# Performance work log

Hardware: AMD Instinct MI355X
Metric: run time of the kernel (lower is better)

## Reference

```python
import jax, jax.numpy as jnp
import numpy as np

B = 4096          # batch
F = 1024          # feature_count * embedding_dim
E = 16            # embedding_dim (domain embedding)
D = 8             # num_domains
T = F + E         # cross-net total dim
L = 3             # cross layers
EPS = 1e-5


def setup_inputs() -> dict:
    key = jax.random.key(0)
    ks = jax.random.split(key, 32)
    s = 0.02
    inp = {}
    inp["x"] = jax.random.normal(ks[0], (B, F), dtype=jnp.float32)
    inp["domain_ids"] = jax.random.randint(ks[1], (B,), 0, D)
    # partitioned normalization params
    inp["pn_weight"] = jnp.ones((D, F), jnp.float32)
    inp["pn_bias"] = jnp.zeros((D, F), jnp.float32)
    # domain embedding table
    inp["dom_emb"] = jax.random.normal(ks[2], (D, E), jnp.float32) * 0.1
    # cross network: L layers, each Linear(T->1, no bias) + additive bias vector
    inp["cross_w"] = jax.random.normal(ks[3], (L, T), jnp.float32) * s
    inp["cross_b"] = jnp.zeros((L, T), jnp.float32)
    # center MLP: T->512->256->128 (ReLU, ReLU, none)
    inp["cW1"] = jax.random.normal(ks[4], (T, 512), jnp.float32) * s
    inp["cb1"] = jnp.zeros((512,), jnp.float32)
    inp["cW2"] = jax.random.normal(ks[5], (512, 256), jnp.float32) * s
    inp["cb2"] = jnp.zeros((256,), jnp.float32)
    inp["cW3"] = jax.random.normal(ks[6], (256, 128), jnp.float32) * s
    inp["cb3"] = jnp.zeros((128,), jnp.float32)
    # per-domain nets: T->512->256->128; last bias initialized to domain_net_init_bias=1.0
    inp["dW1"] = jax.random.normal(ks[7], (D, T, 512), jnp.float32) * s
    inp["db1"] = jnp.zeros((D, 512), jnp.float32)
    inp["dW2"] = jax.random.normal(ks[8], (D, 512, 256), jnp.float32) * s
    inp["db2"] = jnp.zeros((D, 256), jnp.float32)
    inp["dW3"] = jax.random.normal(ks[9], (D, 256, 128), jnp.float32) * s
    inp["db3"] = jnp.ones((D, 128), jnp.float32)
    # final MLP: 128->64->1
    inp["fW1"] = jax.random.normal(ks[10], (128, 64), jnp.float32) * s
    inp["fb1"] = jnp.zeros((64,), jnp.float32)
    inp["fW2"] = jax.random.normal(ks[11], (64, 1), jnp.float32) * s
    inp["fb2"] = jnp.zeros((1,), jnp.float32)
    # auxiliary net: E->32->1
    inp["aW1"] = jax.random.normal(ks[12], (E, 32), jnp.float32) * s
    inp["ab1"] = jnp.zeros((32,), jnp.float32)
    inp["aW2"] = jax.random.normal(ks[13], (32, 1), jnp.float32) * s
    inp["ab2"] = jnp.zeros((1,), jnp.float32)
    return inp


def _forward(x, domain_ids, pn_weight, pn_bias, dom_emb, cross_w, cross_b,
             cW1, cb1, cW2, cb2, cW3, cb3,
             dW1, db1, dW2, db2, dW3, db3,
             fW1, fb1, fW2, fb2, aW1, ab1, aW2, ab2):
    # --- PartitionedNormalization: per-sample LayerNorm stats + domain-indexed affine ---
    mean = jnp.mean(x, axis=1, keepdims=True)
    var = jnp.mean((x - mean) ** 2, axis=1, keepdims=True)  # unbiased=False
    normed = (x - mean) / jnp.sqrt(var + EPS)
    normed = normed * pn_weight[domain_ids] + pn_bias[domain_ids]

    xd = dom_emb[domain_ids]                    # (B, E)
    x0 = jnp.concatenate([normed, xd], axis=1)  # (B, T)

    # --- CrossNetworkWithDomain ---
    xc = x0
    for i in range(L):
        proj = xc @ cross_w[i]                  # (B,)
        xc = x0 * proj[:, None] + cross_b[i] + xc

    # --- center MLP ---
    h = jax.nn.relu(xc @ cW1 + cb1)
    h = jax.nn.relu(h @ cW2 + cb2)
    h_center = h @ cW3 + cb3                    # (B, 128)

    # --- domain-specific nets: run all D nets, select per-sample ---
    a = jax.nn.relu(jnp.einsum('bi,dio->bdo', xc, dW1) + db1[None])   # (B, D, 512)
    a = jax.nn.relu(jnp.einsum('bdi,dio->bdo', a, dW2) + db2[None])   # (B, D, 256)
    a = jnp.einsum('bdi,dio->bdo', a, dW3) + db3[None]                # (B, D, 128)
    h_domain = a[jnp.arange(a.shape[0]), domain_ids]                  # (B, 128)

    # --- STAR fusion (tanh) ---
    fused = h_center * jnp.tanh(h_domain)

    # --- final MLP + auxiliary net ---
    main_logits = jax.nn.relu(fused @ fW1 + fb1) @ fW2 + fb2          # (B, 1)
    aux_logits = jax.nn.relu(xd @ aW1 + ab1) @ aW2 + ab2              # (B, 1)
    return jax.nn.sigmoid(main_logits + aux_logits)


def reference(x, domain_ids, pn_weight, pn_bias, dom_emb, cross_w, cross_b,
              cW1, cb1, cW2, cb2, cW3, cb3,
              dW1, db1, dW2, db2, dW3, db3,
              fW1, fb1, fW2, fb2, aW1, ab1, aW2, ab2):
    return _forward(x, domain_ids, pn_weight, pn_bias, dom_emb, cross_w, cross_b,
                    cW1, cb1, cW2, cb2, cW3, cb3,
                    dW1, db1, dW2, db2, dW3, db3,
                    fW1, fb1, fW2, fb2, aW1, ab1, aW2, ab2)
```

## Files before the change

kernel.cpp:

```cpp
#include <hip/hip_runtime.h>
#include <math.h>
#include <stdint.h>

#define BATCH 4096
#define FEAT  1024
#define EDIM  16
#define NDOM  8
#define TDIM  1040
#define KP1   1088
#define NLAYER 3
#define EPSV  1e-5f

typedef __attribute__((ext_vector_type(8))) short bf16x8;
typedef __attribute__((ext_vector_type(4))) float f32x4;

__device__ __forceinline__ unsigned short f2bf(float f) {
    union { float f; unsigned int u; } v; v.f = f;
    unsigned int u = v.u;
    return (unsigned short)((u + 0x7fffu + ((u >> 16) & 1u)) >> 16);
}
__device__ __forceinline__ float bf2f(unsigned short u) {
    union { unsigned int u; float f; } v; v.u = ((unsigned int)u) << 16; return v.f;
}
__device__ __forceinline__ void gload_lds16(const void* g, void* l) {
    __builtin_amdgcn_global_load_lds(
        (const __attribute__((address_space(1))) void*)(g),
        (__attribute__((address_space(3))) void*)(l), 16, 0, 0);
}

#define T_W1 136
#define T_W2 32
#define T_W3 8
#define NCONV (T_W1*9 + T_W2*9 + T_W3*9)

__global__ __launch_bounds__(256) void convert_group(
    const int* __restrict__ dom, int* __restrict__ perm, int* __restrict__ starts,
    const float* __restrict__ cW1, const float* __restrict__ dW1,
    const float* __restrict__ cW2, const float* __restrict__ dW2,
    const float* __restrict__ cW3, const float* __restrict__ dW3,
    unsigned short* __restrict__ Wc1b, unsigned short* __restrict__ Wd1b,
    unsigned short* __restrict__ Wc2b, unsigned short* __restrict__ Wd2b,
    unsigned short* __restrict__ Wc3b, unsigned short* __restrict__ Wd3b) {
    int b = blockIdx.x;
    int t = threadIdx.x;

    if (b >= NCONV) {
        __shared__ int cnt[NDOM];
        __shared__ int off[NDOM];
        if (t < NDOM) cnt[t] = 0;
        __syncthreads();
        for (int i = t; i < BATCH; i += 256) atomicAdd(&cnt[dom[i]], 1);
        __syncthreads();
        if (t == 0) {
            int s = 0;
            for (int d = 0; d < NDOM; d++) { off[d] = s; starts[d] = s; s += cnt[d]; }
            starts[NDOM] = s;
        }
        __syncthreads();
        for (int i = t; i < BATCH; i += 256) {
            int p = atomicAdd(&off[dom[i]], 1);
            perm[p] = i;
        }
        return;
    }

    __shared__ float tile[64][65];
    const float* src; unsigned short* dst; int K, N, Kp, rr;
    if (b < T_W1)            { src = cW1; dst = Wc1b; K = TDIM; N = 512; Kp = KP1; rr = b; }
    else if (b < T_W1*9)     { int r = b - T_W1; int z = r / T_W1; rr = r % T_W1;
                               src = dW1 + (size_t)z * TDIM * 512; dst = Wd1b + (size_t)z * 512 * KP1;
                               K = TDIM; N = 512; Kp = KP1; }
    else if (b < T_W1*9+T_W2)   { src = cW2; dst = Wc2b; K = 512; N = 256; Kp = 512; rr = b - T_W1*9; }
    else if (b < T_W1*9+T_W2*9) { int r = b - (T_W1*9+T_W2); int z = r / T_W2; rr = r % T_W2;
                               src = dW2 + (size_t)z * 512 * 256; dst = Wd2b + (size_t)z * 256 * 512;
                               K = 512; N = 256; Kp = 512; }
    else if (b < T_W1*9+T_W2*9+T_W3) { src = cW3; dst = Wc3b; K = 256; N = 128; Kp = 256; rr = b - (T_W1*9+T_W2*9); }
    else                     { int r = b - (T_W1*9+T_W2*9+T_W3); int z = r / T_W3; rr = r % T_W3;
                               src = dW3 + (size_t)z * 256 * 128; dst = Wd3b + (size_t)z * 128 * 256;
                               K = 256; N = 128; Kp = 256; }
    int kt = Kp >> 6;
    int kb = rr % kt, nb = rr / kt;
    int k0 = kb * 64, n0 = nb * 64;
    #pragma unroll
    for (int i = 0; i < 4; i++) {
        int flat = t + i * 256;
        int kr = flat >> 4, c4 = flat & 15;
        int k = k0 + kr;
        float4 v = make_float4(0.f, 0.f, 0.f, 0.f);
        if (k < K) v = *(const float4*)(src + (size_t)k * N + n0 + c4 * 4);
        tile[kr][c4 * 4 + 0] = v.x;
        tile[kr][c4 * 4 + 1] = v.y;
        tile[kr][c4 * 4 + 2] = v.z;
        tile[kr][c4 * 4 + 3] = v.w;
    }
    __syncthreads();
    #pragma unroll
    for (int i = 0; i < 4; i++) {
        int flat = t + i * 256;
        int n = flat >> 4, kg = flat & 15;
        ushort4 sv;
        sv.x = f2bf(tile[kg * 4 + 0][n]);
        sv.y = f2bf(tile[kg * 4 + 1][n]);
        sv.z = f2bf(tile[kg * 4 + 2][n]);
        sv.w = f2bf(tile[kg * 4 + 3][n]);
        *(ushort4*)(dst + (size_t)(n0 + n) * Kp + k0 + kg * 4) = sv;
    }
}

__global__ __launch_bounds__(256) void prep_wave(
    const float* __restrict__ x, const int* __restrict__ dom,
    const float* __restrict__ pnw, const float* __restrict__ pnb,
    const float* __restrict__ demb,
    const float* __restrict__ crw, const float* __restrict__ crb,
    const float* __restrict__ aW1, const float* __restrict__ ab1,
    const float* __restrict__ aW2, const float* __restrict__ ab2,
    unsigned short* __restrict__ XCb, float* __restrict__ auxg) {
    int w = threadIdx.x >> 6, lane = threadIdx.x & 63;
    int row = blockIdx.x * 4 + w;
    int d = dom[row];

    float4 X[4];
    #pragma unroll
    for (int j = 0; j < 4; j++)
        X[j] = *(const float4*)(x + (size_t)row * FEAT + 4 * lane + 256 * j);

    float s = 0.f, ss = 0.f;
    #pragma unroll
    for (int j = 0; j < 4; j++) {
        s  += X[j].x + X[j].y + X[j].z + X[j].w;
        ss += X[j].x*X[j].x + X[j].y*X[j].y + X[j].z*X[j].z + X[j].w*X[j].w;
    }
    #pragma unroll
    for (int m = 1; m < 64; m <<= 1) {
        s  += __shfl_xor(s,  m);
        ss += __shfl_xor(ss, m);
    }
    float mean = s / (float)FEAT;
    float var  = ss / (float)FEAT - mean * mean;
    float rstd = rsqrtf(var + EPSV);

    float4 x0[4], xc[4];
    #pragma unroll
    for (int j = 0; j < 4; j++) {
        float4 wv = *(const float4*)(pnw + (size_t)d * FEAT + 4 * lane + 256 * j);
        float4 bv = *(const float4*)(pnb + (size_t)d * FEAT + 4 * lane + 256 * j);
        x0[j].x = (X[j].x - mean) * rstd * wv.x + bv.x;
        x0[j].y = (X[j].y - mean) * rstd * wv.y + bv.y;
        x0[j].z = (X[j].z - mean) * rstd * wv.z + bv.z;
        x0[j].w = (X[j].w - mean) * rstd * wv.w + bv.w;
        xc[j] = x0[j];
    }
    float x0e = 0.f, xce = 0.f;
    if (lane < EDIM) { x0e = demb[d * EDIM + lane]; xce = x0e; }

    #pragma unroll
    for (int l = 0; l < NLAYER; l++) {
        const float* wl = crw + l * TDIM;
        const float* bl = crb + l * TDIM;
        float partial = 0.f;
        #pragma unroll
        for (int j = 0; j < 4; j++) {
            float4 wv = *(const float4*)(wl + 4 * lane + 256 * j);
            partial += xc[j].x*wv.x + xc[j].y*wv.y + xc[j].z*wv.z + xc[j].w*wv.w;
        }
        if (lane < EDIM) partial += xce * wl[FEAT + lane];
        #pragma unroll
        for (int m = 1; m < 64; m <<= 1) partial += __shfl_xor(partial, m);
        float proj = partial;
        #pragma unroll
        for (int j = 0; j < 4; j++) {
            float4 bv = *(const float4*)(bl + 4 * lane + 256 * j);
            xc[j].x = fmaf(x0[j].x, proj, bv.x + xc[j].x);
            xc[j].y = fmaf(x0[j].y, proj, bv.y + xc[j].y);
            xc[j].z = fmaf(x0[j].z, proj, bv.z + xc[j].z);
            xc[j].w = fmaf(x0[j].w, proj, bv.w + xc[j].w);
        }
        if (lane < EDIM) xce = fmaf(x0e, proj, bl[FEAT + lane] + xce);
    }

    #pragma unroll
    for (int j = 0; j < 4; j++) {
        ushort4 sv;
        sv.x = f2bf(xc[j].x); sv.y = f2bf(xc[j].y);
        sv.z = f2bf(xc[j].z); sv.w = f2bf(xc[j].w);
        *(ushort4*)(XCb + (size_t)row * KP1 + 4 * lane + 256 * j) = sv;
    }
    XCb[(size_t)row * KP1 + FEAT + lane] = (lane < EDIM) ? f2bf(xce) : 0;

    float h = (lane < 32) ? ab1[lane] : 0.f;
    #pragma unroll
    for (int e = 0; e < EDIM; e++) {
        float ev = __shfl(xce, e);
        if (lane < 32) h = fmaf(ev, aW1[e * 32 + lane], h);
    }
    float c = (lane < 32) ? fmaxf(h, 0.f) * aW2[lane] : 0.f;
    #pragma unroll
    for (int m = 1; m < 64; m <<= 1) c += __shfl_xor(c, m);
    if (lane == 0) auxg[row] = c + ab2[0];
}

__global__ __launch_bounds__(256) void gemm_mfma_v2(
    const unsigned short* __restrict__ Ac, const unsigned short* __restrict__ Ad, int lda,
    const unsigned short* __restrict__ Wc, const unsigned short* __restrict__ Wd,
    const float* __restrict__ bc, const float* __restrict__ bd,
    unsigned short* __restrict__ Cc, unsigned short* __restrict__ Cd,
    const int* __restrict__ starts, const int* __restrict__ perm, int usePerm,
    int Kp, int N, int relu) {
    __shared__ short As[128 * 64];
    __shared__ short Bs[128 * 64];

    const unsigned short* A; const unsigned short* W; const float* bias;
    unsigned short* C;
    int m0, mEnd;
    int y = blockIdx.y;
    if (y < 32) {
        A = Ac; W = Wc; bias = bc; C = Cc;
        m0 = y * 128; mEnd = BATCH;
    } else {
        int yy = y - 32;
        int d = yy >> 5, sl = yy & 31;
        int ds = starts[d], de = starts[d + 1];
        m0 = ds + sl * 128;
        if (m0 >= de) return;
        mEnd = de;
        A = Ad; W = Wd + (size_t)d * N * Kp; bias = bd + d * N; C = Cd;
    }
    int n0 = blockIdx.x * 128;
    int tid = threadIdx.x;
    int w = tid >> 6, lane = tid & 63;
    int wm = w >> 1, wn = w & 1;
    int lr = lane & 15, q = lane >> 4;

    const unsigned short* pA[4]; const unsigned short* pB[4];
    short* dA[4]; short* dB[4];
    #pragma unroll
    for (int i = 0; i < 4; i++) {
        int seg = i * 4 + w;
        int ch = seg * 64 + lane;
        int loc = ch >> 3, c = ch & 7;
        int mm = m0 + loc; if (mm > mEnd - 1) mm = mEnd - 1;
        int row = usePerm ? perm[mm] : mm;
        pA[i] = A + (size_t)row * lda + ((c ^ (loc & 7)) << 3);
        dA[i] = As + seg * 512;
        pB[i] = W + (size_t)(n0 + loc) * Kp + ((c ^ (loc & 7)) << 3);
        dB[i] = Bs + seg * 512;
    }

    f32x4 acc[4][4];
    #pragma unroll
    for (int i = 0; i < 4; i++)
        #pragma unroll
        for (int j = 0; j < 4; j++)
            acc[i][j] = (f32x4){0.f, 0.f, 0.f, 0.f};

    for (int k0 = 0; k0 < Kp; k0 += 64) {
        #pragma unroll
        for (int i = 0; i < 4; i++) gload_lds16(pA[i] + k0, dA[i]);
        #pragma unroll
        for (int i = 0; i < 4; i++) gload_lds16(pB[i] + k0, dB[i]);
        __syncthreads();

        #pragma unroll
        for (int half = 0; half < 2; half++) {
            int c = half * 4 + q;
            bf16x8 af[4], bf[4];
            #pragma unroll
            for (int i = 0; i < 4; i++) {
                int m = wm * 64 + i * 16 + lr;
                af[i] = *(const bf16x8*)(As + m * 64 + ((c ^ (m & 7)) << 3));
            }
            #pragma unroll
            for (int j = 0; j < 4; j++) {
                int n = wn * 64 + j * 16 + lr;
                bf[j] = *(const bf16x8*)(Bs + n * 64 + ((c ^ (n & 7)) << 3));
            }
            #pragma unroll
            for (int i = 0; i < 4; i++)
                #pragma unroll
                for (int j = 0; j < 4; j++)
                    acc[i][j] = __builtin_amdgcn_mfma_f32_16x16x32_bf16(
                        af[i], bf[j], acc[i][j], 0, 0, 0);
        }
        __syncthreads();
    }

    #pragma unroll
    for (int i = 0; i < 4; i++) {
        #pragma unroll
        for (int j = 0; j < 4; j++) {
            int col = n0 + wn * 64 + j * 16 + lr;
            float bvv = bias[col];
            int rowb = m0 + wm * 64 + i * 16 + q * 4;
            #pragma unroll
            for (int r = 0; r < 4; r++) {
                int row = rowb + r;
                if (row >= mEnd) continue;
                float val = acc[i][j][r] + bvv;
                if (relu) val = fmaxf(val, 0.f);
                C[(size_t)row * N + col] = f2bf(val);
            }
        }
    }
}

__global__ __launch_bounds__(256) void gemm3_final(
    const unsigned short* __restrict__ Ac, const unsigned short* __restrict__ Ad,
    const unsigned short* __restrict__ Wc, const unsigned short* __restrict__ Wd,
    const float* __restrict__ bc, const float* __restrict__ bd,
    const float* __restrict__ fW1, const float* __restrict__ fb1,
    const float* __restrict__ fW2, const float* __restrict__ fb2,
    const float* __restrict__ auxg, const int* __restrict__ perm,
    const int* __restrict__ starts, float* __restrict__ out) {
    __shared__ __align__(16) char smem[40960];
    short* As     = (short*)smem;
    short* Bs     = (short*)(smem + 8192);
    short* fusedB = (short*)(smem + 24576);

    int y = blockIdx.x;
    int d = y >> 6, sl = y & 63;
    int ds = starts[d], de = starts[d + 1];
    int m0 = ds + sl * 64;
    if (m0 >= de) return;
    int mEnd = de;

    int tid = threadIdx.x;
    int w = tid >> 6, lane = tid & 63;
    int wm = w >> 1, wn = w & 1;
    int lr = lane & 15, q = lane >> 4;
    const uint4 zero16 = make_uint4(0u, 0u, 0u, 0u);

    for (int chain = 0; chain < 2; chain++) {
        const unsigned short* A = chain ? Ad : Ac;
        const unsigned short* W = chain ? (Wd + (size_t)d * 128 * 256) : Wc;
        const float* bias = chain ? (bd + d * 128) : bc;
        f32x4 acc[2][4];
        #pragma unroll
        for (int i = 0; i < 2; i++)
            #pragma unroll
            for (int j = 0; j < 4; j++) acc[i][j] = (f32x4){0.f, 0.f, 0.f, 0.f};

        for (int k0 = 0; k0 < 256; k0 += 64) {
            #pragma unroll
            for (int i = 0; i < 2; i++) {
                int flat = tid + i * 256;
                int m = flat >> 3, c = flat & 7;
                int row = m0 + m;
                uint4 val = (row < mEnd)
                    ? *(const uint4*)(A + (size_t)row * 256 + k0 + c * 8) : zero16;
                *(uint4*)(As + m * 64 + ((c ^ (m & 7)) * 8)) = val;
            }
            #pragma unroll
            for (int i = 0; i < 4; i++) {
                int flat = tid + i * 256;
                int n = flat >> 3, c = flat & 7;
                uint4 val = *(const uint4*)(W + (size_t)n * 256 + k0 + c * 8);
                *(uint4*)(Bs + n * 64 + ((c ^ (n & 7)) * 8)) = val;
            }
            __syncthreads();
            #pragma unroll
            for (int g = 0; g < 2; g++) {
                int c = g * 4 + q;
                bf16x8 af[2], bf[4];
                #pragma unroll
                for (int i = 0; i < 2; i++) {
                    int m = wm * 32 + i * 16 + lr;
                    af[i] = *(const bf16x8*)(As + m * 64 + ((c ^ (m & 7)) * 8));
                }
                #pragma unroll
                for (int j = 0; j < 4; j++) {
                    int n = wn * 64 + j * 16 + lr;
                    bf[j] = *(const bf16x8*)(Bs + n * 64 + ((c ^ (n & 7)) * 8));
                }
                #pragma unroll
                for (int i = 0; i < 2; i++)
                    #pragma unroll
                    for (int j = 0; j < 4; j++)
                        acc[i][j] = __builtin_amdgcn_mfma_f32_16x16x32_bf16(
                            af[i], bf[j], acc[i][j], 0, 0, 0);
            }
            __syncthreads();
        }
        #pragma unroll
        for (int i = 0; i < 2; i++) {
            #pragma unroll
            for (int j = 0; j < 4; j++) {
                int col = wn * 64 + j * 16 + lr;
                float bvv = bias[col];
                int cch = col >> 3;
                #pragma unroll
                for (int r = 0; r < 4; r++) {
                    int row = wm * 32 + i * 16 + q * 4 + r;
                    int pc = (cch & 8) | ((cch ^ (row & 7)) & 7);
                    int idx = row * 128 + pc * 8 + (col & 7);
                    if (chain == 0) {
                        fusedB[idx] = (short)f2bf(acc[i][j][r] + bvv);
                    } else {
                        float cv = bf2f((unsigned short)fusedB[idx]);
                        fusedB[idx] = (short)f2bf(cv * tanhf(acc[i][j][r] + bvv));
                    }
                }
            }
        }
    }
    __syncthreads();

    short* Bsf = Bs;
    float* Ls  = (float*)As;
    for (int s2 = tid; s2 < 1024; s2 += 256) {
        int n = s2 >> 4, cch = s2 & 15;
        bf16x8 vv;
        #pragma unroll
        for (int kk = 0; kk < 8; kk++)
            vv[kk] = (short)f2bf(fW1[(cch * 8 + kk) * 64 + n]);
        int pc = (cch & 8) | ((cch ^ (n & 7)) & 7);
        *(bf16x8*)(Bsf + n * 128 + pc * 8) = vv;
    }
    __syncthreads();

    f32x4 acc2[2][2];
    #pragma unroll
    for (int i = 0; i < 2; i++)
        #pragma unroll
        for (int j = 0; j < 2; j++) acc2[i][j] = (f32x4){0.f, 0.f, 0.f, 0.f};
    #pragma unroll
    for (int g = 0; g < 4; g++) {
        int c = g * 4 + q;
        bf16x8 af[2], bf[2];
        #pragma unroll
        for (int i = 0; i < 2; i++) {
            int m = wm * 32 + i * 16 + lr;
            int pc = (c & 8) | ((c ^ (m & 7)) & 7);
            af[i] = *(const bf16x8*)(fusedB + m * 128 + pc * 8);
        }
        #pragma unroll
        for (int j = 0; j < 2; j++) {
            int n = wn * 32 + j * 16 + lr;
            int pc = (c & 8) | ((c ^ (n & 7)) & 7);
            bf[j] = *(const bf16x8*)(Bsf + n * 128 + pc * 8);
        }
        #pragma unroll
        for (int i = 0; i < 2; i++)
            #pragma unroll
            for (int j = 0; j < 2; j++)
                acc2[i][j] = __builtin_amdgcn_mfma_f32_16x16x32_bf16(
                    af[i], bf[j], acc2[i][j], 0, 0, 0);
    }

    float w2v[2], b1v[2];
    #pragma unroll
    for (int j = 0; j < 2; j++) {
        int col = wn * 32 + j * 16 + lr;
        w2v[j] = fW2[col];
        b1v[j] = fb1[col];
    }
    float rowv[2][4];
    #pragma unroll
    for (int i = 0; i < 2; i++)
        #pragma unroll
        for (int r = 0; r < 4; r++) {
            float v = 0.f;
            #pragma unroll
            for (int j = 0; j < 2; j++)
                v += fmaxf(acc2[i][j][r] + b1v[j], 0.f) * w2v[j];
            v += __shfl_xor(v, 1);
            v += __shfl_xor(v, 2);
            v += __shfl_xor(v, 4);
            v += __shfl_xor(v, 8);
            rowv[i][r] = v;
        }
    if (wn == 0 && lr == 0) {
        #pragma unroll
        for (int i = 0; i < 2; i++)
            #pragma unroll
            for (int r = 0; r < 4; r++)
                Ls[wm * 32 + i * 16 + q * 4 + r] = rowv[i][r];
    }
    __syncthreads();
    if (wn == 1 && lr == 0) {
        float b2 = fb2[0];
        #pragma unroll
        for (int i = 0; i < 2; i++)
            #pragma unroll
            for (int r = 0; r < 4; r++) {
                int row = wm * 32 + i * 16 + q * 4 + r;
                int p = m0 + row;
                if (p < mEnd) {
                    int orow = perm[p];
                    float logit = Ls[row] + rowv[i][r] + b2 + auxg[orow];
                    out[orow] = 1.f / (1.f + expf(-logit));
                }
            }
    }
}

extern "C" void kernel_launch(void* const* d_in, const int* in_sizes, int n_in,
                              void* d_out, int out_size, void* d_ws, size_t ws_size,
                              hipStream_t stream) {
    (void)in_sizes; (void)n_in; (void)out_size; (void)ws_size;

    const float* x    = (const float*)d_in[0];
    const int*   dom  = (const int*)  d_in[1];
    const float* pnw  = (const float*)d_in[2];
    const float* pnb  = (const float*)d_in[3];
    const float* demb = (const float*)d_in[4];
    const float* crw  = (const float*)d_in[5];
    const float* crb  = (const float*)d_in[6];
    const float* cW1  = (const float*)d_in[7];
    const float* cb1  = (const float*)d_in[8];
    const float* cW2  = (const float*)d_in[9];
    const float* cb2  = (const float*)d_in[10];
    const float* cW3  = (const float*)d_in[11];
    const float* cb3  = (const float*)d_in[12];
    const float* dW1  = (const float*)d_in[13];
    const float* db1  = (const float*)d_in[14];
    const float* dW2  = (const float*)d_in[15];
    const float* db2  = (const float*)d_in[16];
    const float* dW3  = (const float*)d_in[17];
    const float* db3  = (const float*)d_in[18];
    const float* fW1  = (const float*)d_in[19];
    const float* fb1  = (const float*)d_in[20];
    const float* fW2  = (const float*)d_in[21];
    const float* fb2  = (const float*)d_in[22];
    const float* aW1  = (const float*)d_in[23];
    const float* ab1  = (const float*)d_in[24];
    const float* aW2  = (const float*)d_in[25];
    const float* ab2  = (const float*)d_in[26];
    float* out = (float*)d_out;

    char* base = (char*)d_ws;
    size_t o = 0;
    auto alloc = [&](size_t bytes) { char* p = base + o; o += (bytes + 255) & ~size_t(255); return p; };

    int* perm   = (int*)alloc(BATCH * 4);
    int* starts = (int*)alloc((NDOM + 1) * 4);
    float* auxg = (float*)alloc(BATCH * 4);
    unsigned short* XCb  = (unsigned short*)alloc((size_t)BATCH * KP1 * 2);
    unsigned short* H1c  = (unsigned short*)alloc((size_t)BATCH * 512 * 2);
    unsigned short* H1d  = (unsigned short*)alloc((size_t)BATCH * 512 * 2);
    unsigned short* H2c  = (unsigned short*)alloc((size_t)BATCH * 256 * 2);
    unsigned short* H2d  = (unsigned short*)alloc((size_t)BATCH * 256 * 2);
    unsigned short* Wc1b = (unsigned short*)alloc((size_t)512 * KP1 * 2);
    unsigned short* Wd1b = (unsigned short*)alloc((size_t)NDOM * 512 * KP1 * 2);
    unsigned short* Wc2b = (unsigned short*)alloc((size_t)256 * 512 * 2);
    unsigned short* Wd2b = (unsigned short*)alloc((size_t)NDOM * 256 * 512 * 2);
    unsigned short* Wc3b = (unsigned short*)alloc((size_t)128 * 256 * 2);
    unsigned short* Wd3b = (unsigned short*)alloc((size_t)NDOM * 128 * 256 * 2);

    convert_group<<<NCONV + 1, 256, 0, stream>>>(dom, perm, starts,
                                                 cW1, dW1, cW2, dW2, cW3, dW3,
                                                 Wc1b, Wd1b, Wc2b, Wd2b, Wc3b, Wd3b);
    prep_wave<<<BATCH / 4, 256, 0, stream>>>(x, dom, pnw, pnb, demb, crw, crb,
                                             aW1, ab1, aW2, ab2, XCb, auxg);
    gemm_mfma_v2<<<dim3(512 / 128, 32 + NDOM * 32), 256, 0, stream>>>(
        XCb, XCb, KP1, Wc1b, Wd1b, cb1, db1, H1c, H1d, starts, perm, 1, KP1, 512, 1);
    gemm_mfma_v2<<<dim3(256 / 128, 32 + NDOM * 32), 256, 0, stream>>>(
        H1c, H1d, 512, Wc2b, Wd2b, cb2, db2, H2c, H2d, starts, perm, 0, 512, 256, 1);
    gemm3_final<<<NDOM * 64, 256, 0, stream>>>(
        H2c, H2d, Wc3b, Wd3b, cb3, db3, fW1, fb1, fW2, fb2,
        auxg, perm, starts, out);
}
```

Before: 225.8 us.

## Merge weight conversion with row prep, shrink GEMM N-tile to 64

Folds the weight-conversion/grouping kernel and the per-row normalization/cross-net prep kernel into one launch, so the two independent workloads can run concurrently and one launch boundary goes away. Shrinks the GEMM block tile from 128x128 to 128x64, which doubles the number of workgroups for layers 1 and 2 and improves occupancy and load balance across the 256 CUs, since many domain tiles are partially filled. The trade-off is more A-tile reloads per output and fewer MFMAs per LDS load, which lowers arithmetic intensity.

```diff
diff --git a/kernel.cpp b/kernel.cpp
--- a/kernel.cpp
+++ b/kernel.cpp
@@ -33,18 +33,69 @@
 #define T_W3 8
 #define NCONV (T_W1*9 + T_W2*9 + T_W3*9)
 
-__global__ __launch_bounds__(256) void convert_group(
+__global__ __launch_bounds__(256) void front(
     const int* __restrict__ dom, int* __restrict__ perm, int* __restrict__ starts,
     const float* __restrict__ cW1, const float* __restrict__ dW1,
     const float* __restrict__ cW2, const float* __restrict__ dW2,
     const float* __restrict__ cW3, const float* __restrict__ dW3,
     unsigned short* __restrict__ Wc1b, unsigned short* __restrict__ Wd1b,
     unsigned short* __restrict__ Wc2b, unsigned short* __restrict__ Wd2b,
-    unsigned short* __restrict__ Wc3b, unsigned short* __restrict__ Wd3b) {
+    unsigned short* __restrict__ Wc3b, unsigned short* __restrict__ Wd3b,
+    const float* __restrict__ x,
+    const float* __restrict__ pnw, const float* __restrict__ pnb,
+    const float* __restrict__ demb,
+    const float* __restrict__ crw, const float* __restrict__ crb,
+    const float* __restrict__ aW1, const float* __restrict__ ab1,
+    const float* __restrict__ aW2, const float* __restrict__ ab2,
+    unsigned short* __restrict__ XCb, float* __restrict__ auxg) {
     int b = blockIdx.x;
     int t = threadIdx.x;
 
-    if (b >= NCONV) {
+    if (b < NCONV) {
+        __shared__ float tile[64][65];
+        const float* src; unsigned short* dst; int K, N, Kp, rr;
+        if (b < T_W1)            { src = cW1; dst = Wc1b; K = TDIM; N = 512; Kp = KP1; rr = b; }
+        else if (b < T_W1*9)     { int r = b - T_W1; int z = r / T_W1; rr = r % T_W1;
+                                   src = dW1 + (size_t)z * TDIM * 512; dst = Wd1b + (size_t)z * 512 * KP1;
+                                   K = TDIM; N = 512; Kp = KP1; }
+        else if (b < T_W1*9+T_W2)   { src = cW2; dst = Wc2b; K = 512; N = 256; Kp = 512; rr = b - T_W1*9; }
+        else if (b < T_W1*9+T_W2*9) { int r = b - (T_W1*9+T_W2); int z = r / T_W2; rr = r % T_W2;
+                                   src = dW2 + (size_t)z * 512 * 256; dst = Wd2b + (size_t)z * 256 * 512;
+                                   K = 512; N = 256; Kp = 512; }
+        else if (b < T_W1*9+T_W2*9+T_W3) { src = cW3; dst = Wc3b; K = 256; N = 128; Kp = 256; rr = b - (T_W1*9+T_W2*9); }
+        else                     { int r = b - (T_W1*9+T_W2*9+T_W3); int z = r / T_W3; rr = r % T_W3;
+                                   src = dW3 + (size_t)z * 256 * 128; dst = Wd3b + (size_t)z * 128 * 256;
+                                   K = 256; N = 128; Kp = 256; }
+        int kt = Kp >> 6;
+        int kb = rr % kt, nb = rr / kt;
+        int k0 = kb * 64, n0 = nb * 64;
+        #pragma unroll
+        for (int i = 0; i < 4; i++) {
+            int flat = t + i * 256;
+            int kr = flat >> 4, c4 = flat & 15;
+            int k = k0 + kr;
+            float4 v = make_float4(0.f, 0.f, 0.f, 0.f);
+            if (k < K) v = *(const float4*)(src + (size_t)k * N + n0 + c4 * 4);
+            tile[kr][c4 * 4 + 0] = v.x;
+            tile[kr][c4 * 4 + 1] = v.y;
+            tile[kr][c4 * 4 + 2] = v.z;
+            tile[kr][c4 * 4 + 3] = v.w;
+        }
+        __syncthreads();
+        #pragma unroll
+        for (int i = 0; i < 4; i++) {
+            int flat = t + i * 256;
+            int n = flat >> 4, kg = flat & 15;
+            ushort4 sv;
+            sv.x = f2bf(tile[kg * 4 + 0][n]);
+            sv.y = f2bf(tile[kg * 4 + 1][n]);
+            sv.z = f2bf(tile[kg * 4 + 2][n]);
+            sv.w = f2bf(tile[kg * 4 + 3][n]);
+            *(ushort4*)(dst + (size_t)(n0 + n) * Kp + k0 + kg * 4) = sv;
+        }
+        return;
+    }
+    if (b == NCONV) {
         __shared__ int cnt[NDOM];
         __shared__ int off[NDOM];
         if (t < NDOM) cnt[t] = 0;
@@ -64,59 +115,8 @@
         return;
     }
 
-    __shared__ float tile[64][65];
-    const float* src; unsigned short* dst; int K, N, Kp, rr;
-    if (b < T_W1)            { src = cW1; dst = Wc1b; K = TDIM; N = 512; Kp = KP1; rr = b; }
-    else if (b < T_W1*9)     { int r = b - T_W1; int z = r / T_W1; rr = r % T_W1;
-                               src = dW1 + (size_t)z * TDIM * 512; dst = Wd1b + (size_t)z * 512 * KP1;
-                               K = TDIM; N = 512; Kp = KP1; }
-    else if (b < T_W1*9+T_W2)   { src = cW2; dst = Wc2b; K = 512; N = 256; Kp = 512; rr = b - T_W1*9; }
-    else if (b < T_W1*9+T_W2*9) { int r = b - (T_W1*9+T_W2); int z = r / T_W2; rr = r % T_W2;
-                               src = dW2 + (size_t)z * 512 * 256; dst = Wd2b + (size_t)z * 256 * 512;
-                               K = 512; N = 256; Kp = 512; }
-    else if (b < T_W1*9+T_W2*9+T_W3) { src = cW3; dst = Wc3b; K = 256; N = 128; Kp = 256; rr = b - (T_W1*9+T_W2*9); }
-    else                     { int r = b - (T_W1*9+T_W2*9+T_W3); int z = r / T_W3; rr = r % T_W3;
-                               src = dW3 + (size_t)z * 256 * 128; dst = Wd3b + (size_t)z * 128 * 256;
-                               K = 256; N = 128; Kp = 256; }
-    int kt = Kp >> 6;
-    int kb = rr % kt, nb = rr / kt;
-    int k0 = kb * 64, n0 = nb * 64;
-    #pragma unroll
-    for (int i = 0; i < 4; i++) {
-        int flat = t + i * 256;
-        int kr = flat >> 4, c4 = flat & 15;
-        int k = k0 + kr;
-        float4 v = make_float4(0.f, 0.f, 0.f, 0.f);
-        if (k < K) v = *(const float4*)(src + (size_t)k * N + n0 + c4 * 4);
-        tile[kr][c4 * 4 + 0] = v.x;
-        tile[kr][c4 * 4 + 1] = v.y;
-        tile[kr][c4 * 4 + 2] = v.z;
-        tile[kr][c4 * 4 + 3] = v.w;
-    }
-    __syncthreads();
-    #pragma unroll
-    for (int i = 0; i < 4; i++) {
-        int flat = t + i * 256;
-        int n = flat >> 4, kg = flat & 15;
-        ushort4 sv;
-        sv.x = f2bf(tile[kg * 4 + 0][n]);
-        sv.y = f2bf(tile[kg * 4 + 1][n]);
-        sv.z = f2bf(tile[kg * 4 + 2][n]);
-        sv.w = f2bf(tile[kg * 4 + 3][n]);
-        *(ushort4*)(dst + (size_t)(n0 + n) * Kp + k0 + kg * 4) = sv;
-    }
-}
-
-__global__ __launch_bounds__(256) void prep_wave(
-    const float* __restrict__ x, const int* __restrict__ dom,
-    const float* __restrict__ pnw, const float* __restrict__ pnb,
-    const float* __restrict__ demb,
-    const float* __restrict__ crw, const float* __restrict__ crb,
-    const float* __restrict__ aW1, const float* __restrict__ ab1,
-    const float* __restrict__ aW2, const float* __restrict__ ab2,
-    unsigned short* __restrict__ XCb, float* __restrict__ auxg) {
-    int w = threadIdx.x >> 6, lane = threadIdx.x & 63;
-    int row = blockIdx.x * 4 + w;
+    int w = t >> 6, lane = t & 63;
+    int row = (b - NCONV - 1) * 4 + w;
     int d = dom[row];
 
     float4 X[4];
@@ -199,7 +199,7 @@
     if (lane == 0) auxg[row] = c + ab2[0];
 }
 
-__global__ __launch_bounds__(256) void gemm_mfma_v2(
+__global__ __launch_bounds__(256) void gemm_mfma_v3(
     const unsigned short* __restrict__ Ac, const unsigned short* __restrict__ Ad, int lda,
     const unsigned short* __restrict__ Wc, const unsigned short* __restrict__ Wd,
     const float* __restrict__ bc, const float* __restrict__ bd,
@@ -207,7 +207,7 @@
     const int* __restrict__ starts, const int* __restrict__ perm, int usePerm,
     int Kp, int N, int relu) {
     __shared__ short As[128 * 64];
-    __shared__ short Bs[128 * 64];
+    __shared__ short Bs[64 * 64];
 
     const unsigned short* A; const unsigned short* W; const float* bias;
     unsigned short* C;
@@ -225,59 +225,65 @@
         mEnd = de;
         A = Ad; W = Wd + (size_t)d * N * Kp; bias = bd + d * N; C = Cd;
     }
-    int n0 = blockIdx.x * 128;
+    int n0 = blockIdx.x * 64;
     int tid = threadIdx.x;
     int w = tid >> 6, lane = tid & 63;
     int wm = w >> 1, wn = w & 1;
     int lr = lane & 15, q = lane >> 4;
 
-    const unsigned short* pA[4]; const unsigned short* pB[4];
-    short* dA[4]; short* dB[4];
+    const unsigned short* pA[4]; const unsigned short* pB[2];
+    short* dA[4]; short* dB[2];
     #pragma unroll
     for (int i = 0; i < 4; i++) {
         int seg = i * 4 + w;
         int ch = seg * 64 + lane;
         int loc = ch >> 3, c = ch & 7;
         int mm = m0 + loc; if (mm > mEnd - 1) mm = mEnd - 1;
-        int row = usePerm ? perm[mm] : mm;
-        pA[i] = A + (size_t)row * lda + ((c ^ (loc & 7)) << 3);
+        int rowp = usePerm ? perm[mm] : mm;
+        pA[i] = A + (size_t)rowp * lda + ((c ^ (loc & 7)) << 3);
         dA[i] = As + seg * 512;
+    }
+    #pragma unroll
+    for (int i = 0; i < 2; i++) {
+        int seg = i * 4 + w;
+        int ch = seg * 64 + lane;
+        int loc = ch >> 3, c = ch & 7;
         pB[i] = W + (size_t)(n0 + loc) * Kp + ((c ^ (loc & 7)) << 3);
         dB[i] = Bs + seg * 512;
     }
 
-    f32x4 acc[4][4];
+    f32x4 acc[4][2];
     #pragma unroll
     for (int i = 0; i < 4; i++)
         #pragma unroll
-        for (int j = 0; j < 4; j++)
+        for (int j = 0; j < 2; j++)
             acc[i][j] = (f32x4){0.f, 0.f, 0.f, 0.f};
 
     for (int k0 = 0; k0 < Kp; k0 += 64) {
         #pragma unroll
         for (int i = 0; i < 4; i++) gload_lds16(pA[i] + k0, dA[i]);
         #pragma unroll
-        for (int i = 0; i < 4; i++) gload_lds16(pB[i] + k0, dB[i]);
+        for (int i = 0; i < 2; i++) gload_lds16(pB[i] + k0, dB[i]);
         __syncthreads();
 
         #pragma unroll
         for (int half = 0; half < 2; half++) {
             int c = half * 4 + q;
-            bf16x8 af[4], bf[4];
+            bf16x8 af[4], bf[2];
             #pragma unroll
             for (int i = 0; i < 4; i++) {
                 int m = wm * 64 + i * 16 + lr;
                 af[i] = *(const bf16x8*)(As + m * 64 + ((c ^ (m & 7)) << 3));
             }
             #pragma unroll
-            for (int j = 0; j < 4; j++) {
-                int n = wn * 64 + j * 16 + lr;
+            for (int j = 0; j < 2; j++) {
+                int n = wn * 32 + j * 16 + lr;
                 bf[j] = *(const bf16x8*)(Bs + n * 64 + ((c ^ (n & 7)) << 3));
             }
             #pragma unroll
             for (int i = 0; i < 4; i++)
                 #pragma unroll
-                for (int j = 0; j < 4; j++)
+                for (int j = 0; j < 2; j++)
                     acc[i][j] = __builtin_amdgcn_mfma_f32_16x16x32_bf16(
                         af[i], bf[j], acc[i][j], 0, 0, 0);
         }
@@ -287,8 +293,8 @@
     #pragma unroll
     for (int i = 0; i < 4; i++) {
         #pragma unroll
-        for (int j = 0; j < 4; j++) {
-            int col = n0 + wn * 64 + j * 16 + lr;
+        for (int j = 0; j < 2; j++) {
+            int col = n0 + wn * 32 + j * 16 + lr;
             float bvv = bias[col];
             int rowb = m0 + wm * 64 + i * 16 + q * 4;
             #pragma unroll
@@ -546,15 +552,16 @@
     unsigned short* Wc3b = (unsigned short*)alloc((size_t)128 * 256 * 2);
     unsigned short* Wd3b = (unsigned short*)alloc((size_t)NDOM * 128 * 256 * 2);
 
-    convert_group<<<NCONV + 1, 256, 0, stream>>>(dom, perm, starts,
-                                                 cW1, dW1, cW2, dW2, cW3, dW3,
-                                                 Wc1b, Wd1b, Wc2b, Wd2b, Wc3b, Wd3b);
-    prep_wave<<<BATCH / 4, 256, 0, stream>>>(x, dom, pnw, pnb, demb, crw, crb,
-                                             aW1, ab1, aW2, ab2, XCb, auxg);
-    gemm_mfma_v2<<<dim3(512 / 128, 32 + NDOM * 32), 256, 0, stream>>>(
+    front<<<NCONV + 1 + BATCH / 4, 256, 0, stream>>>(
+        dom, perm, starts, cW1, dW1, cW2, dW2, cW3, dW3,
+        Wc1b, Wd1b, Wc2b, Wd2b, Wc3b, Wd3b,
+        x, pnw, pnb, demb, crw, crb, aW1, ab1, aW2, ab2, XCb, auxg);
+
+    gemm_mfma_v3<<<dim3(512 / 64, 32 + NDOM * 32), 256, 0, stream>>>(
         XCb, XCb, KP1, Wc1b, Wd1b, cb1, db1, H1c, H1d, starts, perm, 1, KP1, 512, 1);
-    gemm_mfma_v2<<<dim3(256 / 128, 32 + NDOM * 32), 256, 0, stream>>>(
+    gemm_mfma_v3<<<dim3(256 / 64, 32 + NDOM * 32), 256, 0, stream>>>(
         H1c, H1d, 512, Wc2b, Wd2b, cb2, db2, H2c, H2d, starts, perm, 0, 512, 256, 1);
+
     gemm3_final<<<NDOM * 64, 256, 0, stream>>>(
         H2c, H2d, Wc3b, Wd3b, cb3, db3, fW1, fb1, fW2, fb2,
         auxg, perm, starts, out);
```

Measured after the change: 216.7 us. 4.1% less time.
